# Performance work log

Measured on AMD Instinct MI355X. Metric: run time of the kernel, lower is better.

## Reference

```python
import jax, jax.numpy as jnp
import numpy as np

B, S, D = 4, 4096, 1024          # batch, seq, in/out features
H = 128                          # controller_hidden_dim
K = 8                            # num_spectral_bases
R = 8                            # low_rank_rank
OR = 8                           # orthogonal_rank
RES_SCALE = 1.0; SPEC_SCALE = 1.0; LR_SCALE = 1.0; ROT_SCALE = 1.0
LN_EPS = 1e-5


def setup_inputs() -> dict:
    key = jax.random.key(0)
    ks = jax.random.split(key, 16)
    g = lambda k, shape, scale=0.02: jax.random.normal(k, shape, jnp.float32) * scale
    return dict(
        x=jax.random.normal(ks[0], (B, S, D), jnp.float32),
        # base linear (teacher-aligned base)
        W_base=g(ks[1], (D, D)), b_base=jnp.zeros((D,), jnp.float32),
        # pooled-token conditioner: LayerNorm -> Linear -> GELU -> Linear
        ln_g=jnp.ones((D,), jnp.float32), ln_b=jnp.zeros((D,), jnp.float32),
        Wc1=g(ks[2], (D, H)), bc1=jnp.zeros((H,), jnp.float32),
        Wc2=g(ks[3], (H, H)), bc2=jnp.zeros((H,), jnp.float32),
        # gate heads
        W_rot_gate=g(ks[4], (H, 1)), b_rot_gate=jnp.zeros((1,), jnp.float32),
        W_rot_coeff=g(ks[5], (H, OR)), b_rot_coeff=jnp.zeros((OR,), jnp.float32),
        W_spec_gate=g(ks[6], (H, K)), b_spec_gate=jnp.zeros((K,), jnp.float32),
        W_lr_coeff=g(ks[7], (H, R)), b_lr_coeff=jnp.zeros((R,), jnp.float32),
        # spectral basis operator: input basis U, output basis V
        U_spec=g(ks[8], (K, D), 0.05), V_spec=g(ks[9], (K, D), 0.05),
        # low-rank residual operator
        U_lr=g(ks[10], (R, D), 0.05), V_lr=g(ks[11], (R, D), 0.05),
        # low-rank orthogonal mixer generators (skew-symmetric pairs)
        A_orth=g(ks[12], (OR, D), 0.05), B_orth=g(ks[13], (OR, D), 0.05),
    )


def reference(x, W_base, b_base, ln_g, ln_b, Wc1, bc1, Wc2, bc2,
              W_rot_gate, b_rot_gate, W_rot_coeff, b_rot_coeff,
              W_spec_gate, b_spec_gate, W_lr_coeff, b_lr_coeff,
              U_spec, V_spec, U_lr, V_lr, A_orth, B_orth):
    # --- pooled token conditioner: mean pool -> LN -> MLP -> hidden h [B,H]
    pooled = x.mean(axis=1)                                   # [B, D]
    mu = pooled.mean(-1, keepdims=True)
    var = pooled.var(-1, keepdims=True)
    z = (pooled - mu) * jax.lax.rsqrt(var + LN_EPS) * ln_g + ln_b
    h = jax.nn.gelu(z @ Wc1 + bc1) @ Wc2 + bc2                # [B, H]

    # --- conditioner-produced gates
    rot_gate = jax.nn.sigmoid(h @ W_rot_gate + b_rot_gate)    # [B, 1]
    rot_coeff = jnp.tanh(h @ W_rot_coeff + b_rot_coeff)       # [B, OR]
    spec_gate = jnp.tanh(h @ W_spec_gate + b_spec_gate)       # [B, K]
    lr_coeff = jnp.tanh(h @ W_lr_coeff + b_lr_coeff)          # [B, R]

    # --- low-rank orthogonal mixer: x_rot = x + gate * x @ G^T,
    #     G = sum_k c_k (a_k b_k^T - b_k a_k^T) (skew-symmetric generator)
    pa = jnp.einsum('bsi,ki->bsk', x, A_orth)
    pb = jnp.einsum('bsi,ki->bsk', x, B_orth)
    rot = (jnp.einsum('bsk,bk,ki->bsi', pb, rot_coeff, A_orth)
           - jnp.einsum('bsk,bk,ki->bsi', pa, rot_coeff, B_orth))
    x_rot = x + (ROT_SCALE * rot_gate)[:, None, :] * rot      # [B,S,D]

    # --- spectral basis operator: gated rank-K map through fixed bases
    s = jnp.einsum('bsi,ki->bsk', x_rot, U_spec)
    y_spec = SPEC_SCALE * jnp.einsum('bsk,bk,ko->bso', s, spec_gate, V_spec)

    # --- low-rank residual operator
    t = jnp.einsum('bsi,ki->bsk', x_rot, U_lr)
    y_lr = LR_SCALE * jnp.einsum('bsk,bk,ko->bso', t, lr_coeff, V_lr)

    # --- teacher-aligned base + gated residual operators
    return x_rot @ W_base + b_base + RES_SCALE * (y_spec + y_lr)
```

## Files before the change

kernel.cpp:

```cpp
#include <hip/hip_runtime.h>

typedef unsigned short u16;
typedef unsigned int   u32;
typedef __bf16 bf16x8 __attribute__((ext_vector_type(8)));
typedef float  f32x4  __attribute__((ext_vector_type(4)));

#define DD 1024

__device__ __forceinline__ u16 f2bf(float f) {
  u32 u = __float_as_uint(f);
  u32 r = (u + 0x7FFFu + ((u >> 16) & 1u)) >> 16;
  return (u16)r;
}

typedef const __attribute__((address_space(1))) void* gp1;
typedef __attribute__((address_space(3))) void* lp3;
__device__ __forceinline__ void gll16(const void* g, void* l) {
  __builtin_amdgcn_global_load_lds((gp1)g, (lp3)l, 16, 0, 0);
}

template <bool XB>
__global__ __launch_bounds__(256) void k01_pre(
    const float* __restrict__ x, u16* __restrict__ xb, float* __restrict__ pooled,
    const float* __restrict__ W,
    const float* __restrict__ Ao, const float* __restrict__ Bo,
    const float* __restrict__ Us, const float* __restrict__ Ul,
    float* __restrict__ AWBW, float* __restrict__ Mbuf,
    u16* __restrict__ Pb, u16* __restrict__ Wt) {
  __shared__ __align__(16) char shb[16384];
  const int tid = threadIdx.x;
  const int bid = blockIdx.x;
  if (bid >= 296) {
    const int i = bid - 296;
    const int xcd = i & 7, local = i >> 3;
    const int rb = xcd * 64 + local;
    const int b = rb >> 7;
    const long r0 = (long)rb * 32;
    const int c0 = tid * 4;
    float s0 = 0.f, s1 = 0.f, s2 = 0.f, s3 = 0.f;
#pragma unroll
    for (int g2 = 0; g2 < 2; g2++) {
      float4 v[16];
#pragma unroll
      for (int r = 0; r < 16; r++)
        v[r] = *(const float4*)(x + (r0 + g2 * 16 + r) * DD + c0);
#pragma unroll
      for (int r = 0; r < 16; r++) {
        if (XB) {
          ushort4 o;
          o.x = f2bf(v[r].x); o.y = f2bf(v[r].y);
          o.z = f2bf(v[r].z); o.w = f2bf(v[r].w);
          *(ushort4*)(xb + (r0 + g2 * 16 + r) * DD + c0) = o;
        }
        s0 += v[r].x; s1 += v[r].y; s2 += v[r].z; s3 += v[r].w;
      }
    }
    atomicAdd(&pooled[b * DD + c0 + 0], s0);
    atomicAdd(&pooled[b * DD + c0 + 1], s1);
    atomicAdd(&pooled[b * DD + c0 + 2], s2);
    atomicAdd(&pooled[b * DD + c0 + 3], s3);
    return;
  }
  if (bid < 32) {
    float (*red2)[128][16] = (float (*)[128][16])shb;
    const int m = bid;
    const int n = (m & 7) * 128 + (tid & 127), q = m >> 3, ih = tid >> 7;
    float acc[16];
#pragma unroll
    for (int k = 0; k < 16; k++) acc[k] = 0.f;
    const int ib = q * 256 + ih * 128;
    for (int i = ib; i < ib + 128; i++) {
      float wv = W[(long)i * DD + n];
#pragma unroll
      for (int k = 0; k < 8; k++) {
        acc[k]     += Ao[k * DD + i] * wv;
        acc[k + 8] += Bo[k * DD + i] * wv;
      }
    }
#pragma unroll
    for (int k = 0; k < 16; k++) red2[ih][tid & 127][k] = acc[k];
    __syncthreads();
    if (ih == 0)
#pragma unroll
      for (int k = 0; k < 16; k++)
        atomicAdd(&AWBW[k * DD + n], red2[0][tid][k] + red2[1][tid][k]);
  } else if (bid < 36) {
    float (*red)[4] = (float (*)[4])shb;
    const int m = bid - 32;
    const float* L  = (m == 0 || m == 2) ? Ao : Bo;
    const float* Rr = (m < 2) ? Us : Ul;
    const int o = tid >> 2, ch = tid & 3;
    const int k = o >> 3, kp = o & 7;
    float a = 0.f;
    for (int i = ch * 256; i < ch * 256 + 256; i++)
      a += L[(long)k * DD + i] * Rr[(long)kp * DD + i];
    red[o][ch] = a;
    __syncthreads();
    if (tid < 64) Mbuf[m * 64 + tid] = red[tid][0] + red[tid][1] + red[tid][2] + red[tid][3];
  } else if (bid < 40) {
    const int m = bid - 36;
    const float* src = m == 0 ? Ao : m == 1 ? Bo : m == 2 ? Us : Ul;
#pragma unroll
    for (int j = 0; j < 8; j++)
      for (int q = 0; q < 4; q++) {
        int i = q * 256 + tid;
        Pb[(m * 8 + j) * DD + i] = f2bf(src[j * DD + i]);
      }
  } else {
    u16 (*T)[66] = (u16 (*)[66])shb;
    const int t = bid - 40, tr = t >> 4, tc = t & 15;
#pragma unroll
    for (int q2 = 0; q2 < 16; q2++) {
      int idx = q2 * 256 + tid, r = idx >> 6, c = idx & 63;
      T[r][c] = f2bf(W[(long)(tr * 64 + r) * DD + tc * 64 + c]);
    }
    __syncthreads();
#pragma unroll
    for (int q2 = 0; q2 < 16; q2++) {
      int idx = q2 * 256 + tid, c = idx >> 6, r = idx & 63;
      Wt[(long)(tc * 64 + c) * DD + tr * 64 + r] = T[r][c];
    }
  }
}

__global__ __launch_bounds__(256) void k2ab(
    const float* __restrict__ pooledsum,
    const float* __restrict__ lng, const float* __restrict__ lnb,
    const float* __restrict__ Wc1, float* __restrict__ h1pre,
    const float* __restrict__ AWBW, const float* Vs, const float* Vl,
    const float* bc1, const float* Wc2, const float* bc2,
    const float* Wrg, const float* brg, const float* Wrc, const float* brc,
    const float* Wsg, const float* bsg, const float* Wlc, const float* blc,
    float* __restrict__ gates, u16* __restrict__ RwT,
    u32* __restrict__ cnt) {
  const int tid = threadIdx.x;
  if (blockIdx.x < 32) {
    __shared__ float zs[1024];
    __shared__ float red[256];
    const int b = blockIdx.x >> 3, ch = blockIdx.x & 7;
    float4 v = *(const float4*)(pooledsum + b * DD + tid * 4);
    v.x *= (1.f / 4096.f); v.y *= (1.f / 4096.f); v.z *= (1.f / 4096.f); v.w *= (1.f / 4096.f);
    float s = v.x + v.y + v.z + v.w;
    float sq = v.x * v.x + v.y * v.y + v.z * v.z + v.w * v.w;
    red[tid] = s; __syncthreads();
    for (int st = 128; st > 0; st >>= 1) { if (tid < st) red[tid] += red[tid + st]; __syncthreads(); }
    float mu = red[0] * (1.f / 1024.f);
    __syncthreads();
    red[tid] = sq; __syncthreads();
    for (int st = 128; st > 0; st >>= 1) { if (tid < st) red[tid] += red[tid + st]; __syncthreads(); }
    float var = red[0] * (1.f / 1024.f) - mu * mu;
    float rs = rsqrtf(var + 1e-5f);
    __syncthreads();
    {
      float4 g = *(const float4*)(lng + tid * 4);
      float4 be = *(const float4*)(lnb + tid * 4);
      zs[tid * 4 + 0] = (v.x - mu) * rs * g.x + be.x;
      zs[tid * 4 + 1] = (v.y - mu) * rs * g.y + be.y;
      zs[tid * 4 + 2] = (v.z - mu) * rs * g.z + be.z;
      zs[tid * 4 + 3] = (v.w - mu) * rs * g.w + be.w;
    }
    __syncthreads();
    const int j = tid & 127, half = tid >> 7;
    float a = 0.f;
#pragma unroll 8
    for (int dd = 0; dd < 64; dd++) {
      int ldi = half * 64 + dd;
      a += zs[ch * 128 + ldi] * Wc1[(long)ch * 16384 + ldi * 128 + j];
    }
    red[tid] = a;
    __syncthreads();
    if (tid < 128) atomicAdd(&h1pre[b * 128 + tid], red[tid] + red[tid + 128]);
    __syncthreads();
    if (tid == 0) atomicAdd(cnt, 1u);
  } else if (blockIdx.x < 36) {
    __shared__ float h1s[128], hb[128];
    __shared__ float red[256];
    const int b = (int)blockIdx.x - 32;
    if (tid == 0) {
      while (atomicAdd(cnt, 0u) < 32u) __builtin_amdgcn_s_sleep(8);
    }
    __syncthreads();
    if (tid < 128) {
      float hv = atomicAdd(&h1pre[b * 128 + tid], 0.f) + bc1[tid];
      float th = tanhf(0.7978845608028654f * (hv + 0.044715f * hv * hv * hv));
      h1s[tid] = 0.5f * hv * (1.f + th);
    }
    __syncthreads();
    const int i = tid & 127, half = tid >> 7;
    float a = 0.f;
#pragma unroll 8
    for (int k = 0; k < 64; k++) {
      int kk = half * 64 + k;
      a += h1s[kk] * Wc2[kk * 128 + i];
    }
    red[tid] = a;
    __syncthreads();
    if (tid < 128) hb[tid] = red[tid] + red[tid + 128] + bc2[tid];
    __syncthreads();
    if (tid < 25) {
      float acc;
      if (tid == 0) {
        acc = brg[0];
        for (int k = 0; k < 128; k++) acc += hb[k] * Wrg[k];
        red[0] = 1.f / (1.f + expf(-acc));
      } else if (tid < 9) {
        int ci = tid - 1; acc = brc[ci];
        for (int k = 0; k < 128; k++) acc += hb[k] * Wrc[k * 8 + ci];
        red[tid] = tanhf(acc);
      } else if (tid < 17) {
        int ci = tid - 9; acc = bsg[ci];
        for (int k = 0; k < 128; k++) acc += hb[k] * Wsg[k * 8 + ci];
        red[tid] = tanhf(acc);
      } else {
        int ci = tid - 17; acc = blc[ci];
        for (int k = 0; k < 128; k++) acc += hb[k] * Wlc[k * 8 + ci];
        red[tid] = tanhf(acc);
      }
    }
    __syncthreads();
    if (tid < 24) {
      float g = red[0];
      gates[b * 32 + tid] = (tid < 8) ? g * red[1 + tid] : red[1 + tid];
    }
  } else {
    const int n = (int)(blockIdx.x - 36) * 256 + tid;
#pragma unroll
    for (int j = 0; j < 8; j++) {
      RwT[n * 32 + j]      = f2bf(AWBW[j * DD + n]);
      RwT[n * 32 + 8 + j]  = f2bf(AWBW[(8 + j) * DD + n]);
      RwT[n * 32 + 16 + j] = f2bf(Vs[(long)j * DD + n]);
      RwT[n * 32 + 24 + j] = f2bf(Vl[(long)j * DD + n]);
    }
  }
}

__global__ __launch_bounds__(256, 2) void k3b_fused(
    const u16* __restrict__ xb, const u16* __restrict__ Wt,
    const u16* __restrict__ Pb, const float* __restrict__ gates,
    const float* __restrict__ Mbuf, const u16* __restrict__ RwT,
    const float* __restrict__ bb, float* __restrict__ out) {
  __shared__ __align__(16) char smem[54400];
  const int tid = threadIdx.x, lane = tid & 63, w = tid >> 6;
  const int quad = lane >> 4, lrow = lane & 15;
  const int g = blockIdx.x;
  const int xcd = g & 7, local = g >> 3;
  const int bm = xcd * 16 + (local >> 2);
  const int bn2 = local & 3;
  const long m0 = (long)bm * 128;
  const int n0 = bn2 * 256;
  const int batch = bm >> 5;
  float* Ml = (float*)(smem + 53248);
  float* gl = (float*)(smem + 54272);
  Ml[tid] = Mbuf[tid];
  if (tid < 24) gl[tid] = gates[batch * 32 + tid];
  const int mw = (w & 1) * 64, nw = (w >> 1) * 128;
  const int pc0 = (w >> 1) * 16;
  const int sr = lane >> 2, sc = (lane & 3) * 16;
  const char* xbp = (const char*)xb;
  const char* wtp = (const char*)Wt;
  const char* pbp = (const char*)Pb;
  const long aOff0 = (m0 + (long)w * 16 + sr) * 2048 + sc;
  const long aOff1 = aOff0 + 64 * 2048;
  const long bOff  = ((long)n0 + w * 16 + sr) * 2048 + sc;
  const long pOff  = ((long)w * 16 + sr) * 2048 + sc;
  const int d0 = w * 1024 + lane * 16;

  f32x4 acc[4][8] = {};
  f32x4 acc2[4] = {};

  gll16(xbp + aOff0, smem + d0);
  gll16(xbp + aOff1, smem + d0 + 4096);
#pragma unroll
  for (int seg = 0; seg < 4; seg++)
    gll16(wtp + bOff + (long)seg * 64 * 2048, smem + 16384 + seg * 4096 + d0);
  if (w < 2) gll16(pbp + pOff, smem + 49152 + d0);
  __syncthreads();

  int cur = 0;
  for (int kc = 0; kc < 32; kc++) {
    if (kc < 31) {
      const long ko = (long)(kc + 1) * 64;
      const int s = cur ^ 1;
      gll16(xbp + aOff0 + ko, smem + s * 8192 + d0);
      gll16(xbp + aOff1 + ko, smem + s * 8192 + d0 + 4096);
#pragma unroll
      for (int seg = 0; seg < 4; seg++)
        gll16(wtp + bOff + (long)seg * 64 * 2048 + ko,
              smem + 16384 + s * 16384 + seg * 4096 + d0);
      if (w < 2) gll16(pbp + pOff + ko, smem + 49152 + s * 2048 + d0);
    }
    const u16* At = (const u16*)(smem + cur * 8192);
    const u16* Bt = (const u16*)(smem + 16384 + cur * 16384);
    const u16* Pt = (const u16*)(smem + 49152 + cur * 2048);
    bf16x8 af[4], bq[8], bp;
#pragma unroll
    for (int tm = 0; tm < 4; tm++)
      af[tm] = *(const bf16x8*)(At + (mw + tm * 16 + lrow) * 32 + quad * 8);
#pragma unroll
    for (int tn = 0; tn < 8; tn++)
      bq[tn] = *(const bf16x8*)(Bt + (nw + tn * 16 + lrow) * 32 + quad * 8);
    bp = *(const bf16x8*)(Pt + (pc0 + lrow) * 32 + quad * 8);
#pragma unroll
    for (int tm = 0; tm < 4; tm++)
#pragma unroll
      for (int tn = 0; tn < 8; tn++)
        acc[tm][tn] = __builtin_amdgcn_mfma_f32_16x16x32_bf16(af[tm], bq[tn], acc[tm][tn], 0, 0, 0);
#pragma unroll
    for (int tm = 0; tm < 4; tm++)
      acc2[tm] = __builtin_amdgcn_mfma_f32_16x16x32_bf16(af[tm], bp, acc2[tm], 0, 0, 0);
    __syncthreads();
    cur ^= 1;
  }

  {
    const long rOff = ((long)n0 + w * 16 + sr) * 64 + sc;
#pragma unroll
    for (int seg = 0; seg < 4; seg++)
      gll16((const char*)RwT + rOff + (long)seg * 64 * 64,
            smem + 16384 + seg * 4096 + d0);
  }
  float* projF = (float*)smem;
#pragma unroll
  for (int tm = 0; tm < 4; tm++)
#pragma unroll
    for (int r = 0; r < 4; r++) {
      int row = mw + tm * 16 + quad * 4 + r;
      int col = pc0 + lrow;
      projF[row * 32 + (col ^ (row & 31))] = acc2[tm][r];
    }
  __syncthreads();
  if (tid < 128) {
    float pr[32];
#pragma unroll
    for (int j = 0; j < 32; j++) pr[j] = projF[tid * 32 + (j ^ (tid & 31))];
    float wo[32];
#pragma unroll
    for (int k = 0; k < 8; k++) { wo[k] = gl[k] * pr[8 + k]; wo[8 + k] = -gl[k] * pr[k]; }
#pragma unroll
    for (int kp = 0; kp < 8; kp++) {
      float sv = pr[16 + kp], tv = pr[24 + kp];
#pragma unroll
      for (int k = 0; k < 8; k++) {
        float gpb = gl[k] * pr[8 + k], gpa = gl[k] * pr[k];
        sv += gpb * Ml[k * 8 + kp]       - gpa * Ml[64 + k * 8 + kp];
        tv += gpb * Ml[128 + k * 8 + kp] - gpa * Ml[192 + k * 8 + kp];
      }
      wo[16 + kp] = gl[8 + kp] * sv;
      wo[24 + kp] = gl[16 + kp] * tv;
    }
    u16* wLds = (u16*)(smem + 32768);
#pragma unroll
    for (int j = 0; j < 32; j++) wLds[tid * 32 + j] = f2bf(wo[j]);
  }
  __syncthreads();
  {
    const u16* wL = (const u16*)(smem + 32768);
    const u16* Rt = (const u16*)(smem + 16384);
    bf16x8 af[4], bq[8];
#pragma unroll
    for (int tm = 0; tm < 4; tm++)
      af[tm] = *(const bf16x8*)(wL + (mw + tm * 16 + lrow) * 32 + quad * 8);
#pragma unroll
    for (int tn = 0; tn < 8; tn++)
      bq[tn] = *(const bf16x8*)(Rt + (nw + tn * 16 + lrow) * 32 + quad * 8);
#pragma unroll
    for (int tm = 0; tm < 4; tm++)
#pragma unroll
      for (int tn = 0; tn < 8; tn++)
        acc[tm][tn] = __builtin_amdgcn_mfma_f32_16x16x32_bf16(af[tm], bq[tn], acc[tm][tn], 0, 0, 0);
  }
#pragma unroll
  for (int tn = 0; tn < 8; tn++) {
    const int col = n0 + nw + tn * 16 + lrow;
    const float bias = bb[col];
#pragma unroll
    for (int tm = 0; tm < 4; tm++)
#pragma unroll
      for (int r = 0; r < 4; r++) {
        long row = m0 + mw + tm * 16 + quad * 4 + r;
        out[row * DD + col] = acc[tm][tn][r] + bias;
      }
  }
}

template <bool XB>
__global__ __launch_bounds__(256) void k3_fused(
    const float* __restrict__ xf, const u16* __restrict__ xb,
    const u16* __restrict__ Wt, const u16* __restrict__ Pb,
    const float* __restrict__ gates, const float* __restrict__ Mbuf,
    const u16* __restrict__ RwT, const float* __restrict__ bb,
    float* __restrict__ out) {
  __shared__ __align__(16) u16 At[4096];
  __shared__ __align__(16) u16 Bt[4096];
  __shared__ __align__(16) u16 Pt[1024];
  __shared__ float projF[128 * 32];
  __shared__ __align__(16) u16 wLds[4096];
  __shared__ float Ml[256];
  __shared__ float gl[24];
  const int tid = threadIdx.x, lane = tid & 63, w = tid >> 6;
  const int quad = lane >> 4, lrow = lane & 15;
  const int bn = blockIdx.x & 7, bm = blockIdx.x >> 3;
  const long m0 = (long)bm * 128;
  const int n0 = bn * 128;
  const int batch = bm >> 5;
  Ml[tid] = Mbuf[tid];
  if (tid < 24) gl[tid] = gates[batch * 32 + tid];
  const int mw = (w & 1) * 64, nw = (w >> 1) * 64;
  const int p0 = (w * 2) * 1024 + lane * 16, p1 = p0 + 1024;
  f32x4 acc[4][4] = {};
  f32x4 acc2[2][2] = {};
  for (int kc = 0; kc < 32; kc++) {
    uint4 vb0 = *(const uint4*)((const char*)Wt + (long)(n0 + (p0 >> 6)) * 2048 + kc * 64 + (p0 & 63));
    uint4 vb1 = *(const uint4*)((const char*)Wt + (long)(n0 + (p1 >> 6)) * 2048 + kc * 64 + (p1 & 63));
    uint4 vp;
    if (tid < 128)
      vp = *(const uint4*)((const char*)Pb + (tid >> 2) * 2048 + kc * 64 + (tid & 3) * 16);
    if (XB) {
      uint4 va0 = *(const uint4*)((const char*)xb + (m0 + (p0 >> 6)) * 2048 + kc * 64 + (p0 & 63));
      uint4 va1 = *(const uint4*)((const char*)xb + (m0 + (p1 >> 6)) * 2048 + kc * 64 + (p1 & 63));
      *(uint4*)((char*)At + p0) = va0;
      *(uint4*)((char*)At + p1) = va1;
    } else {
      ushort4 oa[4];
#pragma unroll
      for (int i = 0; i < 4; i++) {
        int fi = i * 256 + tid, row = fi >> 3, c4 = (fi & 7) * 4;
        float4 v = *(const float4*)(xf + (m0 + row) * DD + kc * 32 + c4);
        oa[i].x = f2bf(v.x); oa[i].y = f2bf(v.y); oa[i].z = f2bf(v.z); oa[i].w = f2bf(v.w);
      }
#pragma unroll
      for (int i = 0; i < 4; i++) {
        int fi = i * 256 + tid, row = fi >> 3, c4 = (fi & 7) * 4;
        *(ushort4*)(At + row * 32 + c4) = oa[i];
      }
    }
    *(uint4*)((char*)Bt + p0) = vb0;
    *(uint4*)((char*)Bt + p1) = vb1;
    if (tid < 128) *(uint4*)((char*)Pt + (tid >> 2) * 64 + (tid & 3) * 16) = vp;
    __syncthreads();
    bf16x8 af[4], bq[4], af2[2], bp[2];
#pragma unroll
    for (int tm = 0; tm < 4; tm++)
      af[tm] = *(const bf16x8*)(At + (mw + tm * 16 + lrow) * 32 + quad * 8);
#pragma unroll
    for (int tn = 0; tn < 4; tn++)
      bq[tn] = *(const bf16x8*)(Bt + (nw + tn * 16 + lrow) * 32 + quad * 8);
#pragma unroll
    for (int t2 = 0; t2 < 2; t2++)
      af2[t2] = *(const bf16x8*)(At + (w * 32 + t2 * 16 + lrow) * 32 + quad * 8);
#pragma unroll
    for (int tn2 = 0; tn2 < 2; tn2++)
      bp[tn2] = *(const bf16x8*)(Pt + (tn2 * 16 + lrow) * 32 + quad * 8);
#pragma unroll
    for (int tm = 0; tm < 4; tm++)
#pragma unroll
      for (int tn = 0; tn < 4; tn++)
        acc[tm][tn] = __builtin_amdgcn_mfma_f32_16x16x32_bf16(af[tm], bq[tn], acc[tm][tn], 0, 0, 0);
#pragma unroll
    for (int t2 = 0; t2 < 2; t2++)
#pragma unroll
      for (int tn2 = 0; tn2 < 2; tn2++)
        acc2[t2][tn2] = __builtin_amdgcn_mfma_f32_16x16x32_bf16(af2[t2], bp[tn2], acc2[t2][tn2], 0, 0, 0);
    __syncthreads();
  }
#pragma unroll
  for (int t2 = 0; t2 < 2; t2++)
#pragma unroll
    for (int tn2 = 0; tn2 < 2; tn2++)
#pragma unroll
      for (int r = 0; r < 4; r++)
        projF[(w * 32 + t2 * 16 + quad * 4 + r) * 32 + tn2 * 16 + lrow] = acc2[t2][tn2][r];
  {
    uint4 vr0 = *(const uint4*)((const char*)RwT + (long)(n0 + (p0 >> 6)) * 64 + (p0 & 63));
    uint4 vr1 = *(const uint4*)((const char*)RwT + (long)(n0 + (p1 >> 6)) * 64 + (p1 & 63));
    *(uint4*)((char*)Bt + p0) = vr0;
    *(uint4*)((char*)Bt + p1) = vr1;
  }
  __syncthreads();
  if (tid < 128) {
    float pr[32];
#pragma unroll
    for (int j = 0; j < 32; j++) pr[j] = projF[tid * 32 + j];
    float wo[32];
#pragma unroll
    for (int k = 0; k < 8; k++) { wo[k] = gl[k] * pr[8 + k]; wo[8 + k] = -gl[k] * pr[k]; }
#pragma unroll
    for (int kp = 0; kp < 8; kp++) {
      float sv = pr[16 + kp], tv = pr[24 + kp];
#pragma unroll
      for (int k = 0; k < 8; k++) {
        float gpb = gl[k] * pr[8 + k], gpa = gl[k] * pr[k];
        sv += gpb * Ml[k * 8 + kp]       - gpa * Ml[64 + k * 8 + kp];
        tv += gpb * Ml[128 + k * 8 + kp] - gpa * Ml[192 + k * 8 + kp];
      }
      wo[16 + kp] = gl[8 + kp] * sv;
      wo[24 + kp] = gl[16 + kp] * tv;
    }
#pragma unroll
    for (int j = 0; j < 32; j++) wLds[tid * 32 + j] = f2bf(wo[j]);
  }
  __syncthreads();
  {
    bf16x8 af[4], bq[4];
#pragma unroll
    for (int tm = 0; tm < 4; tm++)
      af[tm] = *(const bf16x8*)(wLds + (mw + tm * 16 + lrow) * 32 + quad * 8);
#pragma unroll
    for (int tn = 0; tn < 4; tn++)
      bq[tn] = *(const bf16x8*)(Bt + (nw + tn * 16 + lrow) * 32 + quad * 8);
#pragma unroll
    for (int tm = 0; tm < 4; tm++)
#pragma unroll
      for (int tn = 0; tn < 4; tn++)
        acc[tm][tn] = __builtin_amdgcn_mfma_f32_16x16x32_bf16(af[tm], bq[tn], acc[tm][tn], 0, 0, 0);
  }
#pragma unroll
  for (int tn = 0; tn < 4; tn++) {
    const int col = n0 + nw + tn * 16 + lrow;
    const float bias = bb[col];
#pragma unroll
    for (int tm = 0; tm < 4; tm++)
#pragma unroll
      for (int r = 0; r < 4; r++) {
        long row = m0 + mw + tm * 16 + quad * 4 + r;
        out[row * DD + col] = acc[tm][tn][r] + bias;
      }
  }
}

extern "C" void kernel_launch(void* const* d_in, const int* in_sizes, int n_in,
                              void* d_out, int out_size, void* d_ws, size_t ws_size,
                              hipStream_t stream) {
  const float* x   = (const float*)d_in[0];
  const float* Wb  = (const float*)d_in[1];
  const float* bb  = (const float*)d_in[2];
  const float* lng = (const float*)d_in[3];
  const float* lnb = (const float*)d_in[4];
  const float* Wc1 = (const float*)d_in[5];
  const float* bc1 = (const float*)d_in[6];
  const float* Wc2 = (const float*)d_in[7];
  const float* bc2 = (const float*)d_in[8];
  const float* Wrg = (const float*)d_in[9];
  const float* brg = (const float*)d_in[10];
  const float* Wrc = (const float*)d_in[11];
  const float* brc = (const float*)d_in[12];
  const float* Wsg = (const float*)d_in[13];
  const float* bsg = (const float*)d_in[14];
  const float* Wlc = (const float*)d_in[15];
  const float* blc = (const float*)d_in[16];
  const float* Us  = (const float*)d_in[17];
  const float* Vs  = (const float*)d_in[18];
  const float* Ul  = (const float*)d_in[19];
  const float* Vl  = (const float*)d_in[20];
  const float* Ao  = (const float*)d_in[21];
  const float* Bo  = (const float*)d_in[22];

  char* ws = (char*)d_ws;
  float* pooled = (float*)(ws + 0);
  float* AWBW   = (float*)(ws + 16384);
  float* h1pre  = (float*)(ws + 81920);
  float* gates  = (float*)(ws + 83968);
  float* Mbuf   = (float*)(ws + 84480);
  u32*   cntH   = (u32*)  (ws + 85504);
  u16*   RwT    = (u16*)  (ws + 85568);
  u16*   Pb     = (u16*)  (ws + 151104);
  u16*   Wt     = (u16*)  (ws + 216640);
  u16*   xb     = (u16*)  (ws + 2313792);
  float* out    = (float*)d_out;

  const bool modeA = ws_size >= (size_t)2313792 + 33554432;

  (void)hipMemsetAsync(d_ws, 0, 85568, stream);
  if (modeA) {
    k01_pre<true><<<808, 256, 0, stream>>>(x, xb, pooled, Wb, Ao, Bo, Us, Ul,
                                           AWBW, Mbuf, Pb, Wt);
    k2ab<<<40, 256, 0, stream>>>(pooled, lng, lnb, Wc1, h1pre,
                                 AWBW, Vs, Vl, bc1, Wc2, bc2,
                                 Wrg, brg, Wrc, brc, Wsg, bsg, Wlc, blc,
                                 gates, RwT, cntH);
    k3b_fused<<<512, 256, 0, stream>>>(xb, Wt, Pb, gates, Mbuf, RwT, bb, out);
  } else {
    k01_pre<false><<<808, 256, 0, stream>>>(x, xb, pooled, Wb, Ao, Bo, Us, Ul,
                                            AWBW, Mbuf, Pb, Wt);
    k2ab<<<40, 256, 0, stream>>>(pooled, lng, lnb, Wc1, h1pre,
                                 AWBW, Vs, Vl, bc1, Wc2, bc2,
                                 Wrg, brg, Wrc, brc, Wsg, bsg, Wlc, blc,
                                 gates, RwT, cntH);
    k3_fused<false><<<1024, 256, 0, stream>>>(x, xb, Wt, Pb, gates, Mbuf, RwT, bb, out);
  }
}
```

Measured before the change: 295.5 us.

## Merge preprocessing and controller kernels into one launch with atomic-counter dependencies

Folds the controller kernel (LayerNorm/MLP/gate heads and the RwT packing) into the preprocessing kernel. Ordering is enforced with three global atomic counters and spin-waits instead of a kernel boundary. The W-projection work is split across twice as many blocks, and the x-streaming loop now loads 8 rows at a time with a register barrier. The aim is to drop one launch and its tail gap. It relies on the waiting blocks (dispatched after the producers) not starving them, which adds a deadlock risk if block scheduling order changes.

```diff
diff --git a/kernel.cpp b/kernel.cpp
--- a/kernel.cpp
+++ b/kernel.cpp
@@ -20,18 +20,27 @@
 }
 
 template <bool XB>
-__global__ __launch_bounds__(256) void k01_pre(
+__global__ __launch_bounds__(256) void k01m(
     const float* __restrict__ x, u16* __restrict__ xb, float* __restrict__ pooled,
     const float* __restrict__ W,
     const float* __restrict__ Ao, const float* __restrict__ Bo,
     const float* __restrict__ Us, const float* __restrict__ Ul,
     float* __restrict__ AWBW, float* __restrict__ Mbuf,
-    u16* __restrict__ Pb, u16* __restrict__ Wt) {
+    u16* __restrict__ Pb, u16* __restrict__ Wt,
+    const float* __restrict__ lng, const float* __restrict__ lnb,
+    const float* __restrict__ Wc1, float* __restrict__ h1pre,
+    const float* Vs, const float* Vl,
+    const float* bc1, const float* Wc2, const float* bc2,
+    const float* Wrg, const float* brg, const float* Wrc, const float* brc,
+    const float* Wsg, const float* bsg, const float* Wlc, const float* blc,
+    float* __restrict__ gates, u16* __restrict__ RwT,
+    u32* __restrict__ cntS, u32* __restrict__ cntH, u32* __restrict__ cntW) {
   __shared__ __align__(16) char shb[16384];
   const int tid = threadIdx.x;
   const int bid = blockIdx.x;
-  if (bid >= 296) {
-    const int i = bid - 296;
+
+  if (bid >= 328 && bid < 840) {
+    const int i = bid - 328;
     const int xcd = i & 7, local = i >> 3;
     const int rb = xcd * 64 + local;
     const int b = rb >> 7;
@@ -39,37 +48,41 @@
     const int c0 = tid * 4;
     float s0 = 0.f, s1 = 0.f, s2 = 0.f, s3 = 0.f;
 #pragma unroll
-    for (int g2 = 0; g2 < 2; g2++) {
-      float4 v[16];
-#pragma unroll
-      for (int r = 0; r < 16; r++)
-        v[r] = *(const float4*)(x + (r0 + g2 * 16 + r) * DD + c0);
-#pragma unroll
-      for (int r = 0; r < 16; r++) {
+    for (int g2 = 0; g2 < 4; g2++) {
+      f32x4 v[8];
+#pragma unroll
+      for (int r = 0; r < 8; r++)
+        v[r] = *(const f32x4*)(x + (r0 + g2 * 8 + r) * DD + c0);
+      asm volatile("" : "+v"(v[0]), "+v"(v[1]), "+v"(v[2]), "+v"(v[3]),
+                        "+v"(v[4]), "+v"(v[5]), "+v"(v[6]), "+v"(v[7]));
+#pragma unroll
+      for (int r = 0; r < 8; r++) {
         if (XB) {
           ushort4 o;
-          o.x = f2bf(v[r].x); o.y = f2bf(v[r].y);
-          o.z = f2bf(v[r].z); o.w = f2bf(v[r].w);
-          *(ushort4*)(xb + (r0 + g2 * 16 + r) * DD + c0) = o;
+          o.x = f2bf(v[r][0]); o.y = f2bf(v[r][1]);
+          o.z = f2bf(v[r][2]); o.w = f2bf(v[r][3]);
+          *(ushort4*)(xb + (r0 + g2 * 8 + r) * DD + c0) = o;
         }
-        s0 += v[r].x; s1 += v[r].y; s2 += v[r].z; s3 += v[r].w;
+        s0 += v[r][0]; s1 += v[r][1]; s2 += v[r][2]; s3 += v[r][3];
       }
     }
     atomicAdd(&pooled[b * DD + c0 + 0], s0);
     atomicAdd(&pooled[b * DD + c0 + 1], s1);
     atomicAdd(&pooled[b * DD + c0 + 2], s2);
     atomicAdd(&pooled[b * DD + c0 + 3], s3);
+    __syncthreads();
+    if (tid == 0) atomicAdd(cntS, 1u);
     return;
   }
-  if (bid < 32) {
+  if (bid < 64) {
     float (*red2)[128][16] = (float (*)[128][16])shb;
     const int m = bid;
     const int n = (m & 7) * 128 + (tid & 127), q = m >> 3, ih = tid >> 7;
     float acc[16];
 #pragma unroll
     for (int k = 0; k < 16; k++) acc[k] = 0.f;
-    const int ib = q * 256 + ih * 128;
-    for (int i = ib; i < ib + 128; i++) {
+    const int ib = q * 128 + ih * 64;
+    for (int i = ib; i < ib + 64; i++) {
       float wv = W[(long)i * DD + n];
 #pragma unroll
       for (int k = 0; k < 8; k++) {
@@ -84,9 +97,11 @@
 #pragma unroll
       for (int k = 0; k < 16; k++)
         atomicAdd(&AWBW[k * DD + n], red2[0][tid][k] + red2[1][tid][k]);
-  } else if (bid < 36) {
+    __syncthreads();
+    if (tid == 0) atomicAdd(cntW, 1u);
+  } else if (bid < 68) {
     float (*red)[4] = (float (*)[4])shb;
-    const int m = bid - 32;
+    const int m = bid - 64;
     const float* L  = (m == 0 || m == 2) ? Ao : Bo;
     const float* Rr = (m < 2) ? Us : Ul;
     const int o = tid >> 2, ch = tid & 3;
@@ -97,8 +112,8 @@
     red[o][ch] = a;
     __syncthreads();
     if (tid < 64) Mbuf[m * 64 + tid] = red[tid][0] + red[tid][1] + red[tid][2] + red[tid][3];
-  } else if (bid < 40) {
-    const int m = bid - 36;
+  } else if (bid < 72) {
+    const int m = bid - 68;
     const float* src = m == 0 ? Ao : m == 1 ? Bo : m == 2 ? Us : Ul;
 #pragma unroll
     for (int j = 0; j < 8; j++)
@@ -106,9 +121,9 @@
         int i = q * 256 + tid;
         Pb[(m * 8 + j) * DD + i] = f2bf(src[j * DD + i]);
       }
-  } else {
+  } else if (bid < 328) {
     u16 (*T)[66] = (u16 (*)[66])shb;
-    const int t = bid - 40, tr = t >> 4, tc = t & 15;
+    const int t = bid - 72, tr = t >> 4, tc = t & 15;
 #pragma unroll
     for (int q2 = 0; q2 < 16; q2++) {
       int idx = q2 * 256 + tid, r = idx >> 6, c = idx & 63;
@@ -120,25 +135,20 @@
       int idx = q2 * 256 + tid, c = idx >> 6, r = idx & 63;
       Wt[(long)(tc * 64 + c) * DD + tr * 64 + r] = T[r][c];
     }
-  }
-}
-
-__global__ __launch_bounds__(256) void k2ab(
-    const float* __restrict__ pooledsum,
-    const float* __restrict__ lng, const float* __restrict__ lnb,
-    const float* __restrict__ Wc1, float* __restrict__ h1pre,
-    const float* __restrict__ AWBW, const float* Vs, const float* Vl,
-    const float* bc1, const float* Wc2, const float* bc2,
-    const float* Wrg, const float* brg, const float* Wrc, const float* brc,
-    const float* Wsg, const float* bsg, const float* Wlc, const float* blc,
-    float* __restrict__ gates, u16* __restrict__ RwT,
-    u32* __restrict__ cnt) {
-  const int tid = threadIdx.x;
-  if (blockIdx.x < 32) {
-    __shared__ float zs[1024];
-    __shared__ float red[256];
-    const int b = blockIdx.x >> 3, ch = blockIdx.x & 7;
-    float4 v = *(const float4*)(pooledsum + b * DD + tid * 4);
+  } else if (bid < 872) {
+    float* zs  = (float*)shb;
+    float* red = (float*)(shb + 4096);
+    const int lb = bid - 840;
+    const int b = lb >> 3, ch = lb & 7;
+    if (tid == 0) {
+      while (atomicAdd(cntS, 0u) < 512u) __builtin_amdgcn_s_sleep(8);
+    }
+    __syncthreads();
+    float4 v;
+    v.x = atomicAdd(&pooled[b * DD + tid * 4 + 0], 0.f);
+    v.y = atomicAdd(&pooled[b * DD + tid * 4 + 1], 0.f);
+    v.z = atomicAdd(&pooled[b * DD + tid * 4 + 2], 0.f);
+    v.w = atomicAdd(&pooled[b * DD + tid * 4 + 3], 0.f);
     v.x *= (1.f / 4096.f); v.y *= (1.f / 4096.f); v.z *= (1.f / 4096.f); v.w *= (1.f / 4096.f);
     float s = v.x + v.y + v.z + v.w;
     float sq = v.x * v.x + v.y * v.y + v.z * v.z + v.w * v.w;
@@ -171,13 +181,14 @@
     __syncthreads();
     if (tid < 128) atomicAdd(&h1pre[b * 128 + tid], red[tid] + red[tid + 128]);
     __syncthreads();
-    if (tid == 0) atomicAdd(cnt, 1u);
-  } else if (blockIdx.x < 36) {
-    __shared__ float h1s[128], hb[128];
-    __shared__ float red[256];
-    const int b = (int)blockIdx.x - 32;
+    if (tid == 0) atomicAdd(cntH, 1u);
+  } else if (bid < 876) {
+    float* h1s = (float*)shb;
+    float* hb  = (float*)(shb + 512);
+    float* red = (float*)(shb + 1024);
+    const int b = bid - 872;
     if (tid == 0) {
-      while (atomicAdd(cnt, 0u) < 32u) __builtin_amdgcn_s_sleep(8);
+      while (atomicAdd(cntH, 0u) < 32u) __builtin_amdgcn_s_sleep(8);
     }
     __syncthreads();
     if (tid < 128) {
@@ -223,11 +234,15 @@
       gates[b * 32 + tid] = (tid < 8) ? g * red[1 + tid] : red[1 + tid];
     }
   } else {
-    const int n = (int)(blockIdx.x - 36) * 256 + tid;
+    if (tid == 0) {
+      while (atomicAdd(cntW, 0u) < 64u) __builtin_amdgcn_s_sleep(8);
+    }
+    __syncthreads();
+    const int n = (int)(bid - 876) * 256 + tid;
 #pragma unroll
     for (int j = 0; j < 8; j++) {
-      RwT[n * 32 + j]      = f2bf(AWBW[j * DD + n]);
-      RwT[n * 32 + 8 + j]  = f2bf(AWBW[(8 + j) * DD + n]);
+      RwT[n * 32 + j]      = f2bf(atomicAdd(&AWBW[j * DD + n], 0.f));
+      RwT[n * 32 + 8 + j]  = f2bf(atomicAdd(&AWBW[(8 + j) * DD + n], 0.f));
       RwT[n * 32 + 16 + j] = f2bf(Vs[(long)j * DD + n]);
       RwT[n * 32 + 24 + j] = f2bf(Vl[(long)j * DD + n]);
     }
@@ -562,6 +577,8 @@
   float* gates  = (float*)(ws + 83968);
   float* Mbuf   = (float*)(ws + 84480);
   u32*   cntH   = (u32*)  (ws + 85504);
+  u32*   cntS   = (u32*)  (ws + 85508);
+  u32*   cntW   = (u32*)  (ws + 85512);
   u16*   RwT    = (u16*)  (ws + 85568);
   u16*   Pb     = (u16*)  (ws + 151104);
   u16*   Wt     = (u16*)  (ws + 216640);
@@ -572,20 +589,20 @@
 
   (void)hipMemsetAsync(d_ws, 0, 85568, stream);
   if (modeA) {
-    k01_pre<true><<<808, 256, 0, stream>>>(x, xb, pooled, Wb, Ao, Bo, Us, Ul,
-                                           AWBW, Mbuf, Pb, Wt);
-    k2ab<<<40, 256, 0, stream>>>(pooled, lng, lnb, Wc1, h1pre,
-                                 AWBW, Vs, Vl, bc1, Wc2, bc2,
-                                 Wrg, brg, Wrc, brc, Wsg, bsg, Wlc, blc,
-                                 gates, RwT, cntH);
+    k01m<true><<<880, 256, 0, stream>>>(x, xb, pooled, Wb, Ao, Bo, Us, Ul,
+                                        AWBW, Mbuf, Pb, Wt,
+                                        lng, lnb, Wc1, h1pre, Vs, Vl,
+                                        bc1, Wc2, bc2, Wrg, brg, Wrc, brc,
+                                        Wsg, bsg, Wlc, blc, gates, RwT,
+                                        cntS, cntH, cntW);
     k3b_fused<<<512, 256, 0, stream>>>(xb, Wt, Pb, gates, Mbuf, RwT, bb, out);
   } else {
-    k01_pre<false><<<808, 256, 0, stream>>>(x, xb, pooled, Wb, Ao, Bo, Us, Ul,
-                                            AWBW, Mbuf, Pb, Wt);
-    k2ab<<<40, 256, 0, stream>>>(pooled, lng, lnb, Wc1, h1pre,
-                                 AWBW, Vs, Vl, bc1, Wc2, bc2,
-                                 Wrg, brg, Wrc, brc, Wsg, bsg, Wlc, blc,
-                                 gates, RwT, cntH);
+    k01m<false><<<880, 256, 0, stream>>>(x, xb, pooled, Wb, Ao, Bo, Us, Ul,
+                                         AWBW, Mbuf, Pb, Wt,
+                                         lng, lnb, Wc1, h1pre, Vs, Vl,
+                                         bc1, Wc2, bc2, Wrg, brg, Wrc, brc,
+                                         Wsg, bsg, Wlc, blc, gates, RwT,
+                                         cntS, cntH, cntW);
     k3_fused<false><<<1024, 256, 0, stream>>>(x, xb, Wt, Pb, gates, Mbuf, RwT, bb, out);
   }
 }
```

New measurement: 279.4 us. 1.06x faster.
